# Performance work log

Measured on AMD Instinct MI355X. Metric: run time of the kernel, lower is better.

## Reference

```python
import jax, jax.numpy as jnp
import numpy as np

D_MODEL, D_FF, N_EXPERTS, TOP_K = 1024, 4096, 8, 2
BATCH, SEQ = 2, 2048


def setup_inputs() -> dict:
    key = jax.random.key(0)
    ks = jax.random.split(key, 4)
    s_in = 1.0 / np.sqrt(D_MODEL)
    s_ff = 1.0 / np.sqrt(D_FF)
    return {
        "x": jax.random.normal(ks[0], (BATCH, SEQ, D_MODEL), dtype=jnp.float32),
        "Wr": jax.random.normal(ks[1], (D_MODEL, N_EXPERTS), dtype=jnp.float32) * s_in,
        "br": jnp.zeros((N_EXPERTS,), dtype=jnp.float32),
        "W1": jax.random.normal(ks[2], (N_EXPERTS, D_MODEL, D_FF), dtype=jnp.float32) * s_in,
        "b1": jnp.zeros((N_EXPERTS, D_FF), dtype=jnp.float32),
        "W2": jax.random.normal(ks[3], (N_EXPERTS, D_FF, D_MODEL), dtype=jnp.float32) * s_ff,
        "b2": jnp.zeros((N_EXPERTS, D_MODEL), dtype=jnp.float32),
    }


def reference(x, Wr, br, W1, b1, W2, b2):
    B, S, D = x.shape
    E = Wr.shape[1]
    xf = x.reshape(-1, D)  # [T, D]

    # Router: softmax over experts, top-2, renormalize selected weights
    probs = jax.nn.softmax(xf @ Wr + br, axis=-1)            # [T, E]
    top_w, top_i = jax.lax.top_k(probs, TOP_K)               # [T, k]
    top_w = top_w / jnp.sum(top_w, axis=-1, keepdims=True)

    onehot = jax.nn.one_hot(top_i, E, dtype=xf.dtype)        # [T, k, E]
    util = onehot.mean(axis=(0, 1))                          # [E]
    combine = jnp.einsum('tk,tke->te', top_w, onehot)        # [T, E]

    # Grouped expert MLP over all tokens, then weighted combine
    h = jax.nn.gelu(jnp.einsum('td,edf->etf', xf, W1) + b1[:, None, :],
                    approximate=False)                       # [E, T, F]
    y = jnp.einsum('etf,efd->etd', h, W2) + b2[:, None, :]   # [E, T, D]
    out = jnp.einsum('te,etd->td', combine, y).reshape(B, S, D)

    # Aux load-balance loss: squared coefficient of variation (unbiased std)
    cv = jnp.std(util, ddof=1) / (jnp.mean(util) + 1e-6)
    return out, cv ** 2
```

## Files before the change

### kernel.cpp

```cpp
#include <hip/hip_runtime.h>
#include <hip/hip_bf16.h>

#define T_TOK 4096
#define DM 1024
#define DF 4096
#define NE 8

typedef __attribute__((ext_vector_type(4))) float f32x4;
typedef __attribute__((ext_vector_type(8))) short bf16x8;

__device__ inline int swz(int b) { return b ^ ((((b >> 7) ^ (b >> 10)) & 7) << 4); }

__device__ inline unsigned short f2bf(float f) {
  union { float f; unsigned u; } a; a.f = f;
  unsigned r = a.u + 0x7fffu + ((a.u >> 16) & 1u);
  return (unsigned short)(r >> 16);
}
__device__ inline unsigned pk(float lo, float hi) {
  return (unsigned)f2bf(lo) | ((unsigned)f2bf(hi) << 16);
}
__device__ inline float bf2f(unsigned short u) {
  union { unsigned u; float f; } a; a.u = ((unsigned)u) << 16; return a.f;
}

__global__ __launch_bounds__(256) void k_router(const float* __restrict__ x,
    const float* __restrict__ Wr, const float* __restrict__ br,
    int* __restrict__ topi, float* __restrict__ topw, int* __restrict__ counts) {
  int t = blockIdx.x;
  int tid = threadIdx.x;
  const float* xr = x + (size_t)t * DM;
  float acc[NE];
#pragma unroll
  for (int e = 0; e < NE; e++) acc[e] = 0.f;
  for (int d = tid; d < DM; d += 256) {
    float xv = xr[d];
    const float* w = Wr + (size_t)d * NE;
#pragma unroll
    for (int e = 0; e < NE; e++) acc[e] += xv * w[e];
  }
  __shared__ float red[NE][256];
#pragma unroll
  for (int e = 0; e < NE; e++) red[e][tid] = acc[e];
  __syncthreads();
  for (int s = 128; s > 0; s >>= 1) {
    if (tid < s) {
#pragma unroll
      for (int e = 0; e < NE; e++) red[e][tid] += red[e][tid + s];
    }
    __syncthreads();
  }
  if (tid == 0) {
    float l[NE];
#pragma unroll
    for (int e = 0; e < NE; e++) l[e] = red[e][0] + br[e];
    int i0 = 0;
#pragma unroll
    for (int e = 1; e < NE; e++) if (l[e] > l[i0]) i0 = e;
    int i1 = (i0 == 0) ? 1 : 0;
#pragma unroll
    for (int e = 0; e < NE; e++) if (e != i0 && l[e] > l[i1]) i1 = e;
    float w1e = expf(l[i1] - l[i0]);
    float w0 = 1.f / (1.f + w1e);
    topi[2 * t] = i0; topi[2 * t + 1] = i1;
    topw[2 * t] = w0; topw[2 * t + 1] = w1e * w0;
    atomicAdd(&counts[i0], 1);
    atomicAdd(&counts[i1], 1);
  }
}

__global__ void k_scan(const int* __restrict__ counts, int* __restrict__ offsets,
                       float* __restrict__ cv2out) {
  if (threadIdx.x == 0) {
    int off = 0;
    float util[NE];
    for (int e = 0; e < NE; e++) { offsets[e] = off; off += counts[e]; }
    offsets[NE] = off;
    float mean = 0.f;
    for (int e = 0; e < NE; e++) { util[e] = (float)counts[e] / (float)(2 * T_TOK); mean += util[e]; }
    mean *= (1.f / NE);
    float var = 0.f;
    for (int e = 0; e < NE; e++) { float d = util[e] - mean; var += d * d; }
    var *= (1.f / (NE - 1));
    float den = mean + 1e-6f;
    *cv2out = var / (den * den);
  }
}

__global__ __launch_bounds__(256) void k_scatter(const int* __restrict__ topi,
    const float* __restrict__ topw, const int* __restrict__ offsets,
    int* __restrict__ cursor, int* __restrict__ perm, float* __restrict__ permw,
    int* __restrict__ tslot) {
  int t = blockIdx.x * 256 + threadIdx.x;
  if (t >= T_TOK) return;
#pragma unroll
  for (int k = 0; k < 2; k++) {
    int e = topi[2 * t + k];
    int p = atomicAdd(&cursor[e], 1);
    int s = offsets[e] + p;
    perm[s] = t;
    permw[s] = topw[2 * t + k];
    tslot[2 * t + k] = s;
  }
}

__global__ __launch_bounds__(256) void k_gemm1(const float* __restrict__ x,
    const float* __restrict__ W1, const float* __restrict__ b1,
    const int* __restrict__ offsets, const int* __restrict__ perm,
    unsigned short* __restrict__ hb) {
  int e = blockIdx.z;
  int roff = offsets[e];
  int nrows = offsets[e + 1] - roff;
  int row_base = blockIdx.y * 128;
  if (row_base >= nrows) return;
  int n0 = blockIdx.x * 128;
  int tid = threadIdx.x, lane = tid & 63, wid = tid >> 6;
  int wm = (wid >> 1) * 64, wn = (wid & 1) * 64;

  __shared__ __align__(16) char smA[2][16384];
  __shared__ __align__(16) char smB[2][16384];
  __shared__ int tok_s[128];
  if (tid < 128) { int r = row_base + tid; tok_s[tid] = (r < nrows) ? perm[roff + r] : -1; }
  __syncthreads();

  const float* W1e = W1 + (size_t)e * DM * DF;

  f32x4 acc[4][4];
#pragma unroll
  for (int m = 0; m < 4; m++)
#pragma unroll
    for (int n = 0; n < 4; n++) acc[m][n] = (f32x4)(0.f);

  float4 arA[4][2];
  float4 brB[8];
  int aRow[4], aG[4];
#pragma unroll
  for (int i = 0; i < 4; i++) { int q = i * 256 + tid; aRow[i] = q >> 3; aG[i] = q & 7; }
  int bn4 = tid & 31, bk8 = tid >> 5;

  auto STAGE = [&](int kk) {
    int k0 = kk * 64;
#pragma unroll
    for (int i = 0; i < 4; i++) {
      int tk = tok_s[aRow[i]];
      if (tk >= 0) {
        const float* p = x + (size_t)tk * DM + k0 + aG[i] * 8;
        arA[i][0] = *(const float4*)p;
        arA[i][1] = *(const float4*)(p + 4);
      } else {
        arA[i][0] = make_float4(0, 0, 0, 0);
        arA[i][1] = make_float4(0, 0, 0, 0);
      }
    }
    const float* bp = W1e + (size_t)(k0 + bk8 * 8) * DF + n0 + bn4 * 4;
#pragma unroll
    for (int j = 0; j < 8; j++) brB[j] = *(const float4*)(bp + (size_t)j * DF);
  };
  auto WRITE = [&](int p) {
#pragma unroll
    for (int i = 0; i < 4; i++) {
      uint4 v;
      v.x = pk(arA[i][0].x, arA[i][0].y);
      v.y = pk(arA[i][0].z, arA[i][0].w);
      v.z = pk(arA[i][1].x, arA[i][1].y);
      v.w = pk(arA[i][1].z, arA[i][1].w);
      *(uint4*)(smA[p] + swz(aRow[i] * 128 + aG[i] * 16)) = v;
    }
#pragma unroll
    for (int c = 0; c < 4; c++) {
      uint4 v;
      v.x = pk(brB[0][c], brB[1][c]);
      v.y = pk(brB[2][c], brB[3][c]);
      v.z = pk(brB[4][c], brB[5][c]);
      v.w = pk(brB[6][c], brB[7][c]);
      int row = bn4 * 4 + c;
      *(uint4*)(smB[p] + swz(row * 128 + bk8 * 16)) = v;
    }
  };
  auto COMPUTE = [&](int p) {
#pragma unroll
    for (int ks = 0; ks < 2; ks++) {
      bf16x8 af[4], bfr[4];
#pragma unroll
      for (int m = 0; m < 4; m++) {
        int row = wm + m * 16 + (lane & 15);
        af[m] = *(const bf16x8*)(smA[p] + swz(row * 128 + ks * 64 + (lane >> 4) * 16));
      }
#pragma unroll
      for (int n = 0; n < 4; n++) {
        int col = wn + n * 16 + (lane & 15);
        bfr[n] = *(const bf16x8*)(smB[p] + swz(col * 128 + ks * 64 + (lane >> 4) * 16));
      }
#pragma unroll
      for (int m = 0; m < 4; m++)
#pragma unroll
        for (int n = 0; n < 4; n++)
          acc[m][n] = __builtin_amdgcn_mfma_f32_16x16x32_bf16(af[m], bfr[n], acc[m][n], 0, 0, 0);
    }
  };

  STAGE(0); WRITE(0); __syncthreads();
  for (int kk = 0; kk < DM / 64; kk++) {
    if (kk < DM / 64 - 1) STAGE(kk + 1);
    COMPUTE(kk & 1);
    if (kk < DM / 64 - 1) WRITE((kk + 1) & 1);
    __syncthreads();
  }

#pragma unroll
  for (int n = 0; n < 4; n++) {
    int col = n0 + wn + n * 16 + (lane & 15);
    float b1v = b1[e * DF + col];
#pragma unroll
    for (int m = 0; m < 4; m++) {
      int rbase = wm + m * 16 + ((lane >> 4) << 2);
#pragma unroll
      for (int r = 0; r < 4; r++) {
        int grow = row_base + rbase + r;
        if (grow < nrows) {
          float v = acc[m][n][r] + b1v;
          float g = 0.5f * v * (1.f + erff(v * 0.70710678118f));
          hb[(size_t)(roff + grow) * DF + col] = f2bf(g);
        }
      }
    }
  }
}

__global__ __launch_bounds__(256) void k_gemm2(const unsigned short* __restrict__ hb,
    const float* __restrict__ W2, const int* __restrict__ offsets,
    unsigned short* __restrict__ y) {
  int e = blockIdx.z;
  int roff = offsets[e];
  int nrows = offsets[e + 1] - roff;
  int row_base = blockIdx.y * 128;
  if (row_base >= nrows) return;
  int n0 = blockIdx.x * 128;
  int tid = threadIdx.x, lane = tid & 63, wid = tid >> 6;
  int wm = (wid >> 1) * 64, wn = (wid & 1) * 64;

  __shared__ __align__(16) char smA[2][16384];
  __shared__ __align__(16) char smB[2][16384];

  const float* W2e = W2 + (size_t)e * DF * DM;

  f32x4 acc[4][4];
#pragma unroll
  for (int m = 0; m < 4; m++)
#pragma unroll
    for (int n = 0; n < 4; n++) acc[m][n] = (f32x4)(0.f);

  uint4 arA[4];
  float4 brB[8];
  int aRow[4], aG[4];
#pragma unroll
  for (int i = 0; i < 4; i++) { int q = i * 256 + tid; aRow[i] = q >> 3; aG[i] = q & 7; }
  int bn4 = tid & 31, bk8 = tid >> 5;

  auto STAGE = [&](int kk) {
    int k0 = kk * 64;
#pragma unroll
    for (int i = 0; i < 4; i++) {
      int r = row_base + aRow[i];
      if (r < nrows)
        arA[i] = *(const uint4*)(hb + (size_t)(roff + r) * DF + k0 + aG[i] * 8);
      else
        arA[i] = make_uint4(0, 0, 0, 0);
    }
    const float* bp = W2e + (size_t)(k0 + bk8 * 8) * DM + n0 + bn4 * 4;
#pragma unroll
    for (int j = 0; j < 8; j++) brB[j] = *(const float4*)(bp + (size_t)j * DM);
  };
  auto WRITE = [&](int p) {
#pragma unroll
    for (int i = 0; i < 4; i++)
      *(uint4*)(smA[p] + swz(aRow[i] * 128 + aG[i] * 16)) = arA[i];
#pragma unroll
    for (int c = 0; c < 4; c++) {
      uint4 v;
      v.x = pk(brB[0][c], brB[1][c]);
      v.y = pk(brB[2][c], brB[3][c]);
      v.z = pk(brB[4][c], brB[5][c]);
      v.w = pk(brB[6][c], brB[7][c]);
      int row = bn4 * 4 + c;
      *(uint4*)(smB[p] + swz(row * 128 + bk8 * 16)) = v;
    }
  };
  auto COMPUTE = [&](int p) {
#pragma unroll
    for (int ks = 0; ks < 2; ks++) {
      bf16x8 af[4], bfr[4];
#pragma unroll
      for (int m = 0; m < 4; m++) {
        int row = wm + m * 16 + (lane & 15);
        af[m] = *(const bf16x8*)(smA[p] + swz(row * 128 + ks * 64 + (lane >> 4) * 16));
      }
#pragma unroll
      for (int n = 0; n < 4; n++) {
        int col = wn + n * 16 + (lane & 15);
        bfr[n] = *(const bf16x8*)(smB[p] + swz(col * 128 + ks * 64 + (lane >> 4) * 16));
      }
#pragma unroll
      for (int m = 0; m < 4; m++)
#pragma unroll
        for (int n = 0; n < 4; n++)
          acc[m][n] = __builtin_amdgcn_mfma_f32_16x16x32_bf16(af[m], bfr[n], acc[m][n], 0, 0, 0);
    }
  };

  STAGE(0); WRITE(0); __syncthreads();
  for (int kk = 0; kk < DF / 64; kk++) {
    if (kk < DF / 64 - 1) STAGE(kk + 1);
    COMPUTE(kk & 1);
    if (kk < DF / 64 - 1) WRITE((kk + 1) & 1);
    __syncthreads();
  }

#pragma unroll
  for (int m = 0; m < 4; m++) {
    int rbase = wm + m * 16 + ((lane >> 4) << 2);
#pragma unroll
    for (int r = 0; r < 4; r++) {
      int grow = row_base + rbase + r;
      if (grow < nrows) {
#pragma unroll
        for (int n = 0; n < 4; n++) {
          int col = n0 + wn + n * 16 + (lane & 15);
          y[(size_t)(roff + grow) * DM + col] = f2bf(acc[m][n][r]);
        }
      }
    }
  }
}

__global__ __launch_bounds__(256) void k_combine(const int* __restrict__ topi,
    const float* __restrict__ topw, const int* __restrict__ tslot,
    const unsigned short* __restrict__ y, const float* __restrict__ b2,
    float* __restrict__ out) {
  int t = blockIdx.x, tid = threadIdx.x;
  int s0 = tslot[2 * t], s1 = tslot[2 * t + 1];
  int e0 = topi[2 * t], e1 = topi[2 * t + 1];
  float w0 = topw[2 * t], w1 = topw[2 * t + 1];
  int d = tid * 4;
  uint2 ya = *(const uint2*)(y + (size_t)s0 * DM + d);
  uint2 yb = *(const uint2*)(y + (size_t)s1 * DM + d);
  f32x4 bb0 = *(const f32x4*)(b2 + (size_t)e0 * DM + d);
  f32x4 bb1 = *(const f32x4*)(b2 + (size_t)e1 * DM + d);
  f32x4 r;
  r[0] = w0 * (bf2f((unsigned short)(ya.x & 0xffff)) + bb0[0]) + w1 * (bf2f((unsigned short)(yb.x & 0xffff)) + bb1[0]);
  r[1] = w0 * (bf2f((unsigned short)(ya.x >> 16)) + bb0[1]) + w1 * (bf2f((unsigned short)(yb.x >> 16)) + bb1[1]);
  r[2] = w0 * (bf2f((unsigned short)(ya.y & 0xffff)) + bb0[2]) + w1 * (bf2f((unsigned short)(yb.y & 0xffff)) + bb1[2]);
  r[3] = w0 * (bf2f((unsigned short)(ya.y >> 16)) + bb0[3]) + w1 * (bf2f((unsigned short)(yb.y >> 16)) + bb1[3]);
  *(f32x4*)(out + (size_t)t * DM + d) = r;
}

extern "C" void kernel_launch(void* const* d_in, const int* in_sizes, int n_in,
                              void* d_out, int out_size, void* d_ws, size_t ws_size,
                              hipStream_t stream) {
  const float* x  = (const float*)d_in[0];
  const float* Wr = (const float*)d_in[1];
  const float* br = (const float*)d_in[2];
  const float* W1 = (const float*)d_in[3];
  const float* b1 = (const float*)d_in[4];
  const float* W2 = (const float*)d_in[5];
  const float* b2 = (const float*)d_in[6];
  float* out = (float*)d_out;

  char* ws = (char*)d_ws;
  int*   counts  = (int*)(ws + 0);
  int*   cursor  = (int*)(ws + 64);
  int*   offsets = (int*)(ws + 128);
  int*   topi    = (int*)(ws + 256);
  float* topw    = (float*)(ws + 33024);
  int*   perm    = (int*)(ws + 65792);
  float* permw   = (float*)(ws + 98560);
  int*   tslot   = (int*)(ws + 131328);
  unsigned short* hb = (unsigned short*)(ws + 164096);
  unsigned short* y  = (unsigned short*)(ws + 164096 + 67108864);

  hipMemsetAsync(ws, 0, 256, stream);

  k_router<<<T_TOK, 256, 0, stream>>>(x, Wr, br, topi, topw, counts);
  k_scan<<<1, 64, 0, stream>>>(counts, offsets, out + (size_t)T_TOK * DM);
  k_scatter<<<16, 256, 0, stream>>>(topi, topw, offsets, cursor, perm, permw, tslot);
  k_gemm1<<<dim3(32, 32, 8), 256, 0, stream>>>(x, W1, b1, offsets, perm, hb);
  k_gemm2<<<dim3(8, 32, 8), 256, 0, stream>>>(hb, W2, offsets, y);
  k_combine<<<T_TOK, 256, 0, stream>>>(topi, topw, tslot, y, b2, out);
}
```

Measured before the change: 803.2 us.

## Pre-convert inputs to transposed bf16 and stream GEMM tiles via global_load_lds

Adds per-call conversion kernels: one turns x into bf16, and one transposes W1 and W2 into bf16 K-contiguous layouts. Both expert GEMMs then copy 16-byte chunks straight from global memory into XOR-swizzled LDS with global_load_lds. This removes the in-loop fp32 loads, register packing and LDS writes from the GEMM main loops. In exchange it adds extra full passes over the weight tensors on every call, and drops the register-staged double buffering for a single LDS buffer with two barriers per k-step. Padded rows now read valid but irrelevant data instead of being zero-filled.

Measured after the change: 784.2 us. 1.02x faster.

```diff
diff --git a/kernel.cpp b/kernel.cpp
--- a/kernel.cpp
+++ b/kernel.cpp
@@ -9,8 +9,6 @@
 typedef __attribute__((ext_vector_type(4))) float f32x4;
 typedef __attribute__((ext_vector_type(8))) short bf16x8;
 
-__device__ inline int swz(int b) { return b ^ ((((b >> 7) ^ (b >> 10)) & 7) << 4); }
-
 __device__ inline unsigned short f2bf(float f) {
   union { float f; unsigned u; } a; a.f = f;
   unsigned r = a.u + 0x7fffu + ((a.u >> 16) & 1u);
@@ -21,6 +19,12 @@
 }
 __device__ inline float bf2f(unsigned short u) {
   union { unsigned u; float f; } a; a.u = ((unsigned)u) << 16; return a.f;
+}
+
+__device__ inline void gload16(const void* g, void* l) {
+  __builtin_amdgcn_global_load_lds(
+      (const __attribute__((address_space(1))) unsigned int*)g,
+      (__attribute__((address_space(3))) unsigned int*)l, 16, 0, 0);
 }
 
 __global__ __launch_bounds__(256) void k_router(const float* __restrict__ x,
@@ -87,9 +91,8 @@
 }
 
 __global__ __launch_bounds__(256) void k_scatter(const int* __restrict__ topi,
-    const float* __restrict__ topw, const int* __restrict__ offsets,
-    int* __restrict__ cursor, int* __restrict__ perm, float* __restrict__ permw,
-    int* __restrict__ tslot) {
+    const int* __restrict__ offsets, int* __restrict__ cursor,
+    int* __restrict__ perm, int* __restrict__ tslot) {
   int t = blockIdx.x * 256 + threadIdx.x;
   if (t >= T_TOK) return;
 #pragma unroll
@@ -98,13 +101,48 @@
     int p = atomicAdd(&cursor[e], 1);
     int s = offsets[e] + p;
     perm[s] = t;
-    permw[s] = topw[2 * t + k];
     tslot[2 * t + k] = s;
   }
 }
 
-__global__ __launch_bounds__(256) void k_gemm1(const float* __restrict__ x,
-    const float* __restrict__ W1, const float* __restrict__ b1,
+__global__ __launch_bounds__(256) void k_cvtx(const float* __restrict__ x,
+    unsigned short* __restrict__ xc) {
+  size_t i = ((size_t)blockIdx.x * 256 + threadIdx.x) * 8;
+  f32x4 a = *(const f32x4*)(x + i);
+  f32x4 b = *(const f32x4*)(x + i + 4);
+  uint4 v;
+  v.x = pk(a[0], a[1]); v.y = pk(a[2], a[3]);
+  v.z = pk(b[0], b[1]); v.w = pk(b[2], b[3]);
+  *(uint4*)(xc + i) = v;
+}
+
+__global__ __launch_bounds__(256) void k_cvtT(const float* __restrict__ src,
+    unsigned short* __restrict__ dst, int K, int N) {
+  int e = blockIdx.z;
+  int n0 = blockIdx.x * 64, k0 = blockIdx.y * 64;
+  int tid = threadIdx.x;
+  __shared__ float tile[64][65];
+  const float* s = src + (size_t)e * K * N + (size_t)k0 * N + n0;
+  int r0 = tid >> 4, c4 = (tid & 15) * 4;
+#pragma unroll
+  for (int i = 0; i < 4; i++) {
+    int r = r0 + i * 16;
+    float4 v = *(const float4*)(s + (size_t)r * N + c4);
+    tile[r][c4] = v.x; tile[r][c4 + 1] = v.y; tile[r][c4 + 2] = v.z; tile[r][c4 + 3] = v.w;
+  }
+  __syncthreads();
+  int n = tid >> 2, kc = (tid & 3) * 16;
+  unsigned o[8];
+#pragma unroll
+  for (int j = 0; j < 8; j++)
+    o[j] = pk(tile[kc + 2 * j][n], tile[kc + 2 * j + 1][n]);
+  unsigned short* dp = dst + (size_t)e * N * K + (size_t)(n0 + n) * K + k0 + kc;
+  *(uint4*)dp = make_uint4(o[0], o[1], o[2], o[3]);
+  *(uint4*)(dp + 8) = make_uint4(o[4], o[5], o[6], o[7]);
+}
+
+__global__ __launch_bounds__(256) void k_gemm1(const unsigned short* __restrict__ xc,
+    const unsigned short* __restrict__ W1t, const float* __restrict__ b1,
     const int* __restrict__ offsets, const int* __restrict__ perm,
     unsigned short* __restrict__ hb) {
   int e = blockIdx.z;
@@ -116,79 +154,60 @@
   int tid = threadIdx.x, lane = tid & 63, wid = tid >> 6;
   int wm = (wid >> 1) * 64, wn = (wid & 1) * 64;
 
-  __shared__ __align__(16) char smA[2][16384];
-  __shared__ __align__(16) char smB[2][16384];
+  __shared__ __align__(16) unsigned short smA[128 * 64];
+  __shared__ __align__(16) unsigned short smB[128 * 64];
   __shared__ int tok_s[128];
-  if (tid < 128) { int r = row_base + tid; tok_s[tid] = (r < nrows) ? perm[roff + r] : -1; }
+  if (tid < 128) {
+    int r = row_base + tid;
+    tok_s[tid] = (r < nrows) ? perm[roff + r] : 0;
+  }
   __syncthreads();
 
-  const float* W1e = W1 + (size_t)e * DM * DF;
-
   f32x4 acc[4][4];
 #pragma unroll
   for (int m = 0; m < 4; m++)
 #pragma unroll
     for (int n = 0; n < 4; n++) acc[m][n] = (f32x4)(0.f);
 
-  float4 arA[4][2];
-  float4 brB[8];
-  int aRow[4], aG[4];
-#pragma unroll
-  for (int i = 0; i < 4; i++) { int q = i * 256 + tid; aRow[i] = q >> 3; aG[i] = q & 7; }
-  int bn4 = tid & 31, bk8 = tid >> 5;
-
-  auto STAGE = [&](int kk) {
+  const unsigned short* Bbase = W1t + (size_t)e * DF * DM + (size_t)n0 * DM;
+
+  const unsigned short* aP[4];
+  const unsigned short* bP[4];
+  unsigned short* lA[4];
+  unsigned short* lB[4];
+#pragma unroll
+  for (int i = 0; i < 4; i++) {
+    int c = tid + i * 256;
+    int row = c >> 3;
+    int o = ((c & 7) ^ (row & 7)) * 8;
+    aP[i] = xc + (size_t)tok_s[row] * DM + o;
+    bP[i] = Bbase + (size_t)row * DM + o;
+    lA[i] = smA + c * 8;
+    lB[i] = smB + c * 8;
+  }
+
+  for (int kk = 0; kk < DM / 64; kk++) {
     int k0 = kk * 64;
 #pragma unroll
     for (int i = 0; i < 4; i++) {
-      int tk = tok_s[aRow[i]];
-      if (tk >= 0) {
-        const float* p = x + (size_t)tk * DM + k0 + aG[i] * 8;
-        arA[i][0] = *(const float4*)p;
-        arA[i][1] = *(const float4*)(p + 4);
-      } else {
-        arA[i][0] = make_float4(0, 0, 0, 0);
-        arA[i][1] = make_float4(0, 0, 0, 0);
-      }
-    }
-    const float* bp = W1e + (size_t)(k0 + bk8 * 8) * DF + n0 + bn4 * 4;
-#pragma unroll
-    for (int j = 0; j < 8; j++) brB[j] = *(const float4*)(bp + (size_t)j * DF);
-  };
-  auto WRITE = [&](int p) {
-#pragma unroll
-    for (int i = 0; i < 4; i++) {
-      uint4 v;
-      v.x = pk(arA[i][0].x, arA[i][0].y);
-      v.y = pk(arA[i][0].z, arA[i][0].w);
-      v.z = pk(arA[i][1].x, arA[i][1].y);
-      v.w = pk(arA[i][1].z, arA[i][1].w);
-      *(uint4*)(smA[p] + swz(aRow[i] * 128 + aG[i] * 16)) = v;
-    }
-#pragma unroll
-    for (int c = 0; c < 4; c++) {
-      uint4 v;
-      v.x = pk(brB[0][c], brB[1][c]);
-      v.y = pk(brB[2][c], brB[3][c]);
-      v.z = pk(brB[4][c], brB[5][c]);
-      v.w = pk(brB[6][c], brB[7][c]);
-      int row = bn4 * 4 + c;
-      *(uint4*)(smB[p] + swz(row * 128 + bk8 * 16)) = v;
-    }
-  };
-  auto COMPUTE = [&](int p) {
+      gload16(aP[i] + k0, lA[i]);
+      gload16(bP[i] + k0, lB[i]);
+    }
+    __syncthreads();
 #pragma unroll
     for (int ks = 0; ks < 2; ks++) {
       bf16x8 af[4], bfr[4];
 #pragma unroll
       for (int m = 0; m < 4; m++) {
         int row = wm + m * 16 + (lane & 15);
-        af[m] = *(const bf16x8*)(smA[p] + swz(row * 128 + ks * 64 + (lane >> 4) * 16));
+        int col = ks * 64 + (lane >> 4) * 16;
+        af[m] = *(const bf16x8*)((const char*)smA + row * 128 + (col ^ ((row & 7) << 4)));
       }
 #pragma unroll
       for (int n = 0; n < 4; n++) {
-        int col = wn + n * 16 + (lane & 15);
-        bfr[n] = *(const bf16x8*)(smB[p] + swz(col * 128 + ks * 64 + (lane >> 4) * 16));
+        int row = wn + n * 16 + (lane & 15);
+        int col = ks * 64 + (lane >> 4) * 16;
+        bfr[n] = *(const bf16x8*)((const char*)smB + row * 128 + (col ^ ((row & 7) << 4)));
       }
 #pragma unroll
       for (int m = 0; m < 4; m++)
@@ -196,13 +215,6 @@
         for (int n = 0; n < 4; n++)
           acc[m][n] = __builtin_amdgcn_mfma_f32_16x16x32_bf16(af[m], bfr[n], acc[m][n], 0, 0, 0);
     }
-  };
-
-  STAGE(0); WRITE(0); __syncthreads();
-  for (int kk = 0; kk < DM / 64; kk++) {
-    if (kk < DM / 64 - 1) STAGE(kk + 1);
-    COMPUTE(kk & 1);
-    if (kk < DM / 64 - 1) WRITE((kk + 1) & 1);
     __syncthreads();
   }
 
@@ -227,7 +239,7 @@
 }
 
 __global__ __launch_bounds__(256) void k_gemm2(const unsigned short* __restrict__ hb,
-    const float* __restrict__ W2, const int* __restrict__ offsets,
+    const unsigned short* __restrict__ W2t, const int* __restrict__ offsets,
     unsigned short* __restrict__ y) {
   int e = blockIdx.z;
   int roff = offsets[e];
@@ -238,10 +250,8 @@
   int tid = threadIdx.x, lane = tid & 63, wid = tid >> 6;
   int wm = (wid >> 1) * 64, wn = (wid & 1) * 64;
 
-  __shared__ __align__(16) char smA[2][16384];
-  __shared__ __align__(16) char smB[2][16384];
-
-  const float* W2e = W2 + (size_t)e * DF * DM;
+  __shared__ __align__(16) unsigned short smA[128 * 64];
+  __shared__ __align__(16) unsigned short smB[128 * 64];
 
   f32x4 acc[4][4];
 #pragma unroll
@@ -249,55 +259,46 @@
 #pragma unroll
     for (int n = 0; n < 4; n++) acc[m][n] = (f32x4)(0.f);
 
-  uint4 arA[4];
-  float4 brB[8];
-  int aRow[4], aG[4];
-#pragma unroll
-  for (int i = 0; i < 4; i++) { int q = i * 256 + tid; aRow[i] = q >> 3; aG[i] = q & 7; }
-  int bn4 = tid & 31, bk8 = tid >> 5;
-
-  auto STAGE = [&](int kk) {
+  const unsigned short* Abase = hb + (size_t)(roff + row_base) * DF;
+  const unsigned short* Bbase = W2t + (size_t)e * DM * DF + (size_t)n0 * DF;
+
+  const unsigned short* aP[4];
+  const unsigned short* bP[4];
+  unsigned short* lA[4];
+  unsigned short* lB[4];
+#pragma unroll
+  for (int i = 0; i < 4; i++) {
+    int c = tid + i * 256;
+    int row = c >> 3;
+    int o = ((c & 7) ^ (row & 7)) * 8;
+    aP[i] = Abase + (size_t)row * DF + o;
+    bP[i] = Bbase + (size_t)row * DF + o;
+    lA[i] = smA + c * 8;
+    lB[i] = smB + c * 8;
+  }
+
+  for (int kk = 0; kk < DF / 64; kk++) {
     int k0 = kk * 64;
 #pragma unroll
     for (int i = 0; i < 4; i++) {
-      int r = row_base + aRow[i];
-      if (r < nrows)
-        arA[i] = *(const uint4*)(hb + (size_t)(roff + r) * DF + k0 + aG[i] * 8);
-      else
-        arA[i] = make_uint4(0, 0, 0, 0);
-    }
-    const float* bp = W2e + (size_t)(k0 + bk8 * 8) * DM + n0 + bn4 * 4;
-#pragma unroll
-    for (int j = 0; j < 8; j++) brB[j] = *(const float4*)(bp + (size_t)j * DM);
-  };
-  auto WRITE = [&](int p) {
-#pragma unroll
-    for (int i = 0; i < 4; i++)
-      *(uint4*)(smA[p] + swz(aRow[i] * 128 + aG[i] * 16)) = arA[i];
-#pragma unroll
-    for (int c = 0; c < 4; c++) {
-      uint4 v;
-      v.x = pk(brB[0][c], brB[1][c]);
-      v.y = pk(brB[2][c], brB[3][c]);
-      v.z = pk(brB[4][c], brB[5][c]);
-      v.w = pk(brB[6][c], brB[7][c]);
-      int row = bn4 * 4 + c;
-      *(uint4*)(smB[p] + swz(row * 128 + bk8 * 16)) = v;
-    }
-  };
-  auto COMPUTE = [&](int p) {
+      gload16(aP[i] + k0, lA[i]);
+      gload16(bP[i] + k0, lB[i]);
+    }
+    __syncthreads();
 #pragma unroll
     for (int ks = 0; ks < 2; ks++) {
       bf16x8 af[4], bfr[4];
 #pragma unroll
       for (int m = 0; m < 4; m++) {
         int row = wm + m * 16 + (lane & 15);
-        af[m] = *(const bf16x8*)(smA[p] + swz(row * 128 + ks * 64 + (lane >> 4) * 16));
+        int col = ks * 64 + (lane >> 4) * 16;
+        af[m] = *(const bf16x8*)((const char*)smA + row * 128 + (col ^ ((row & 7) << 4)));
       }
 #pragma unroll
       for (int n = 0; n < 4; n++) {
-        int col = wn + n * 16 + (lane & 15);
-        bfr[n] = *(const bf16x8*)(smB[p] + swz(col * 128 + ks * 64 + (lane >> 4) * 16));
+        int row = wn + n * 16 + (lane & 15);
+        int col = ks * 64 + (lane >> 4) * 16;
+        bfr[n] = *(const bf16x8*)((const char*)smB + row * 128 + (col ^ ((row & 7) << 4)));
       }
 #pragma unroll
       for (int m = 0; m < 4; m++)
@@ -305,13 +306,6 @@
         for (int n = 0; n < 4; n++)
           acc[m][n] = __builtin_amdgcn_mfma_f32_16x16x32_bf16(af[m], bfr[n], acc[m][n], 0, 0, 0);
     }
-  };
-
-  STAGE(0); WRITE(0); __syncthreads();
-  for (int kk = 0; kk < DF / 64; kk++) {
-    if (kk < DF / 64 - 1) STAGE(kk + 1);
-    COMPUTE(kk & 1);
-    if (kk < DF / 64 - 1) WRITE((kk + 1) & 1);
     __syncthreads();
   }
 
@@ -372,17 +366,22 @@
   int*   topi    = (int*)(ws + 256);
   float* topw    = (float*)(ws + 33024);
   int*   perm    = (int*)(ws + 65792);
-  float* permw   = (float*)(ws + 98560);
-  int*   tslot   = (int*)(ws + 131328);
-  unsigned short* hb = (unsigned short*)(ws + 164096);
-  unsigned short* y  = (unsigned short*)(ws + 164096 + 67108864);
+  int*   tslot   = (int*)(ws + 98560);
+  unsigned short* xc  = (unsigned short*)(ws + 164096);
+  unsigned short* hb  = (unsigned short*)(ws + 8552704);
+  unsigned short* y   = (unsigned short*)(ws + 75661568);
+  unsigned short* W1t = (unsigned short*)(ws + 92438784);
+  unsigned short* W2t = (unsigned short*)(ws + 159547648);
 
   hipMemsetAsync(ws, 0, 256, stream);
 
+  k_cvtx<<<T_TOK * DM / (256 * 8), 256, 0, stream>>>(x, xc);
+  k_cvtT<<<dim3(DF / 64, DM / 64, NE), 256, 0, stream>>>(W1, W1t, DM, DF);
+  k_cvtT<<<dim3(DM / 64, DF / 64, NE), 256, 0, stream>>>(W2, W2t, DF, DM);
   k_router<<<T_TOK, 256, 0, stream>>>(x, Wr, br, topi, topw, counts);
   k_scan<<<1, 64, 0, stream>>>(counts, offsets, out + (size_t)T_TOK * DM);
-  k_scatter<<<16, 256, 0, stream>>>(topi, topw, offsets, cursor, perm, permw, tslot);
-  k_gemm1<<<dim3(32, 32, 8), 256, 0, stream>>>(x, W1, b1, offsets, perm, hb);
-  k_gemm2<<<dim3(8, 32, 8), 256, 0, stream>>>(hb, W2, offsets, y);
+  k_scatter<<<16, 256, 0, stream>>>(topi, offsets, cursor, perm, tslot);
+  k_gemm1<<<dim3(32, 32, 8), 256, 0, stream>>>(xc, W1t, b1, offsets, perm, hb);
+  k_gemm2<<<dim3(8, 32, 8), 256, 0, stream>>>(hb, W2t, offsets, y);
   k_combine<<<T_TOK, 256, 0, stream>>>(topi, topw, tslot, y, b2, out);
 }
```
